# Optimization experiments

Hardware: AMD Instinct MI355X
Metric: run time of the kernel (lower is better)

Reference implementation:

```python
import jax, jax.numpy as jnp
import numpy as np
from jax import lax

V, E, H, L = 32000, 1024, 512, 2
B, S, TL = 32, 128, 63  # batch, src_len, label_len; trg_len = TL+1 = 64
START, PAD = 1, 0
NEG = -1e10


def setup_inputs() -> dict:
    key = jax.random.key(0)
    ks = iter(jax.random.split(key, 40))
    def w(shape):
        return jax.random.normal(next(ks), shape, jnp.float32) * 0.01
    inp = {
        'input_ids': jax.random.randint(next(ks), (B, S), 0, V),
        'attention_mask': jnp.ones((B, S), jnp.int32),
        'labels': jax.random.randint(next(ks), (B, TL), 0, V),
        # encoder params (bidirectional GRU; layer0 input dim E == 2H so stackable)
        'enc_emb': w((V, E)),
        'enc_Wih': w((L, 2, 3 * H, 2 * H)),
        'enc_Whh': w((L, 2, 3 * H, H)),
        'enc_bih': jnp.zeros((L, 2, 3 * H), jnp.float32),
        'enc_bhh': jnp.zeros((L, 2, 3 * H), jnp.float32),
        'fc_W': w((L, H, 2 * H)),
        'fc_b': jnp.zeros((L, H), jnp.float32),
        # attention
        'attn_W': w((H, 3 * H)),
        'attn_b': jnp.zeros((H,), jnp.float32),
        'attn_v': w((H,)),
        # decoder
        'dec_emb': w((V, E)),
        'dec_Wih0': w((3 * H, E + 2 * H)),
        'dec_Wihr': w((L - 1, 3 * H, H)),
        'dec_Whh': w((L, 3 * H, H)),
        'dec_bih': jnp.zeros((L, 3 * H), jnp.float32),
        'dec_bhh': jnp.zeros((L, 3 * H), jnp.float32),
        'out_W': w((V, H + 2 * H + E)),
        'out_b': jnp.zeros((V,), jnp.float32),
    }
    return inp


def gru_cell(x, h, Wih, Whh, bih, bhh):
    gi = x @ Wih.T + bih
    gh = h @ Whh.T + bhh
    i_r, i_z, i_n = jnp.split(gi, 3, axis=-1)
    h_r, h_z, h_n = jnp.split(gh, 3, axis=-1)
    r = jax.nn.sigmoid(i_r + h_r)
    z = jax.nn.sigmoid(i_z + h_z)
    n = jnp.tanh(i_n + r * h_n)
    return (1.0 - z) * n + z * h


def run_dir(x_seq, m_seq, Wih, Whh, bih, bhh, reverse):
    # x_seq: [S,B,D], m_seq: [S,B,1] bool. Emulates pack_padded: hidden freezes
    # past each sequence's length; padded outputs are zero.
    h0 = jnp.zeros((x_seq.shape[1], H), x_seq.dtype)
    def step(h, xm):
        x_t, m_t = xm
        hn = gru_cell(x_t, h, Wih, Whh, bih, bhh)
        return jnp.where(m_t, hn, h), jnp.where(m_t, hn, 0.0)
    hF, outs = lax.scan(step, h0, (x_seq, m_seq), reverse=reverse)
    return outs, hF


def reference(input_ids, attention_mask, labels, enc_emb, enc_Wih, enc_Whh,
              enc_bih, enc_bhh, fc_W, fc_b, attn_W, attn_b, attn_v, dec_emb,
              dec_Wih0, dec_Wihr, dec_Whh, dec_bih, dec_bhh, out_W, out_b):
    src = input_ids.T                                   # [S,B]
    m_sb = (attention_mask.T != 0)[:, :, None]          # [S,B,1]
    x = enc_emb[src]                                    # [S,B,E]
    ff = bf = None
    for l in range(L):
        fo, ff = run_dir(x, m_sb, enc_Wih[l, 0], enc_Whh[l, 0], enc_bih[l, 0], enc_bhh[l, 0], False)
        bo, bf = run_dir(x, m_sb, enc_Wih[l, 1], enc_Whh[l, 1], enc_bih[l, 1], enc_bhh[l, 1], True)
        x = jnp.concatenate([fo, bo], axis=-1)          # [S,B,2H]
    enc_out = x                                         # [S,B,2H]
    fc_in = jnp.concatenate([ff, bf], axis=-1)          # [B,2H]
    hidden = jnp.stack([jnp.tanh(fc_in @ fc_W[l].T + fc_b[l]) for l in range(L)])  # [L,B,H]

    # teacher forcing ratio = 1.0 -> always use target token
    trg = jnp.concatenate([jnp.full((1, B), START, labels.dtype),
                           jnp.where(labels.T == -100, PAD, labels.T)], axis=0)  # [T,B]
    tokens = trg[:-1]                                   # [T-1,B]

    enc_b = enc_out.transpose(1, 0, 2)                  # [B,S,2H]
    mask_b = (attention_mask != 0)                      # [B,S]

    def dec_step(hid, tok):
        emb = dec_emb[tok]                              # [B,E]
        h_top = hid[-1]                                 # [B,H]
        feat = jnp.concatenate(
            [jnp.broadcast_to(h_top[:, None, :], (B, S, H)), enc_b], axis=-1)
        energy = jnp.tanh(feat @ attn_W.T + attn_b)     # [B,S,H]
        scores = jnp.where(mask_b, energy @ attn_v, NEG)
        a = jax.nn.softmax(scores, axis=1)              # [B,S]
        weighted = jnp.einsum('bs,bsd->bd', a, enc_b)   # [B,2H]
        x_l = jnp.concatenate([emb, weighted], axis=-1)
        new_h = []
        h0n = gru_cell(x_l, hid[0], dec_Wih0, dec_Whh[0], dec_bih[0], dec_bhh[0])
        new_h.append(h0n)
        x_l = h0n
        for l in range(1, L):
            hln = gru_cell(x_l, hid[l], dec_Wihr[l - 1], dec_Whh[l], dec_bih[l], dec_bhh[l])
            new_h.append(hln)
            x_l = hln
        pred = jnp.concatenate([x_l, weighted, emb], axis=-1) @ out_W.T + out_b
        return jnp.stack(new_h), pred

    _, preds = lax.scan(dec_step, hidden, tokens)       # [T-1,B,V]
    logits = jnp.concatenate([jnp.zeros((1, B, V), preds.dtype), preds], axis=0)
    return logits.transpose(1, 0, 2)                    # [B,T,V]
```

## Files before the change

### kernel.cpp

```cpp
#include <hip/hip_runtime.h>
#include <hip/hip_bf16.h>

#define V 32000
#define E 1024
#define H 512
#define NL 2
#define B_ 32
#define S_ 128
#define TL_ 63

typedef __attribute__((ext_vector_type(8))) short short8;
typedef __attribute__((ext_vector_type(4))) float f32x4;

__device__ __forceinline__ float sigmoidf_(float x){ return 1.f/(1.f + __expf(-x)); }
__device__ __forceinline__ float fast_tanh(float x){ return 1.f - 2.f/(__expf(2.f*x) + 1.f); }
__device__ __forceinline__ ushort f2bf_(float f){
  uint u = __builtin_bit_cast(uint, f);
  uint r = (u + 0x7FFFu + ((u >> 16) & 1u)) >> 16;
  return (ushort)r;
}

__device__ __forceinline__ float aload(const float* p){
  return __hip_atomic_load(p, __ATOMIC_RELAXED, __HIP_MEMORY_SCOPE_SYSTEM);
}
__device__ __forceinline__ void astore(float* p, float v){
  __hip_atomic_store(p, v, __ATOMIC_RELAXED, __HIP_MEMORY_SCOPE_SYSTEM);
}

__device__ __forceinline__ void gbar(uint* ctr, uint* gen, uint nblk, uint e){
  __syncthreads();
  if (threadIdx.x == 0){
    uint old = __hip_atomic_fetch_add(ctr, 1u, __ATOMIC_RELAXED, __HIP_MEMORY_SCOPE_SYSTEM);
    if (old == e*nblk - 1u){
      __hip_atomic_store(gen, e, __ATOMIC_RELAXED, __HIP_MEMORY_SCOPE_SYSTEM);
    } else {
      while (__hip_atomic_load(gen, __ATOMIC_RELAXED, __HIP_MEMORY_SCOPE_SYSTEM) < e)
        __builtin_amdgcn_s_sleep(2);
    }
  }
  __syncthreads();
}

__global__ __launch_bounds__(256) void embed_enc(const int* __restrict__ ids,
                                                 const float* __restrict__ emb,
                                                 float* __restrict__ X0){
  int row = blockIdx.x;
  int s = row >> 5, b = row & 31;
  int tok = ids[b*S_ + s];
  const float4* src = (const float4*)(emb + (size_t)tok*E);
  float4* dst = (float4*)(X0 + (size_t)row*E);
  dst[threadIdx.x] = src[threadIdx.x];
}

__global__ __launch_bounds__(256) void embed_dec(const int* __restrict__ labels,
                                                 const float* __restrict__ emb,
                                                 float* __restrict__ Feat){
  int row = blockIdx.x;
  int t = row >> 5, b = row & 31;
  int tok = (t == 0) ? 1 : labels[b*TL_ + (t-1)];
  if (tok == -100) tok = 0;
  const float4* src = (const float4*)(emb + (size_t)tok*E);
  float4* dst = (float4*)(Feat + (size_t)row*2560 + 1536);
  dst[threadIdx.x] = src[threadIdx.x];
}

__global__ __launch_bounds__(256) void gemm_f32(
    const float* __restrict__ A, int lda,
    const float* __restrict__ B, int ldb,
    const float* __restrict__ bias,
    float* __restrict__ C, int ldc,
    int M, int N, int K)
{
  __shared__ float As[8][132];
  __shared__ float Bs[8][132];
  int tid = threadIdx.x;
  int row0 = blockIdx.x*128, col0 = blockIdx.y*128;
  int lr = tid >> 1;
  int lk = (tid & 1) * 4;
  int ar = row0 + lr; if (ar > M-1) ar = M-1;
  const float* Ap = A + (size_t)ar*lda + lk;
  const float* Bp = B + (size_t)(col0 + lr)*ldb + lk;
  int tx = tid & 15, ty = tid >> 4;
  float acc[8][8];
  #pragma unroll
  for (int i=0;i<8;i++){
    #pragma unroll
    for (int j=0;j<8;j++) acc[i][j]=0.f;
  }
  for (int k0 = 0; k0 < K; k0 += 8){
    float4 a = *(const float4*)(Ap + k0);
    float4 b = *(const float4*)(Bp + k0);
    __syncthreads();
    As[lk+0][lr]=a.x; As[lk+1][lr]=a.y; As[lk+2][lr]=a.z; As[lk+3][lr]=a.w;
    Bs[lk+0][lr]=b.x; Bs[lk+1][lr]=b.y; Bs[lk+2][lr]=b.z; Bs[lk+3][lr]=b.w;
    __syncthreads();
    #pragma unroll
    for (int k=0;k<8;k++){
      float av[8], bv[8];
      *(float4*)&av[0] = *(const float4*)&As[k][ty*8];
      *(float4*)&av[4] = *(const float4*)&As[k][ty*8+4];
      *(float4*)&bv[0] = *(const float4*)&Bs[k][tx*8];
      *(float4*)&bv[4] = *(const float4*)&Bs[k][tx*8+4];
      #pragma unroll
      for (int i=0;i<8;i++){
        #pragma unroll
        for (int j=0;j<8;j++) acc[i][j] += av[i]*bv[j];
      }
    }
  }
  #pragma unroll
  for (int i=0;i<8;i++){
    int r = row0 + ty*8 + i;
    if (r < M){
      float* Cp = C + (size_t)r*ldc + col0 + tx*8;
      #pragma unroll
      for (int j=0;j<8;j++) Cp[j] = acc[i][j] + bias[col0 + tx*8 + j];
    }
  }
}

__global__ __launch_bounds__(256) void enc_layer(
    const float* __restrict__ GIf, const float* __restrict__ GIbk,
    const float* __restrict__ Whh, const float* __restrict__ bhh,
    const int* __restrict__ amask,
    float* __restrict__ hFa, float* __restrict__ hFb,
    float* __restrict__ hBa, float* __restrict__ hBb,
    float* __restrict__ Xout, uint* __restrict__ barbase)
{
  int dir  = blockIdx.x >> 7;
  int rr   = blockIdx.x & 127;
  int bg   = rr >> 4;
  int jblk = rr & 15;
  uint* z   = barbase + (size_t)(dir*8 + bg)*512;
  uint* ctr = z; uint* gen = z + 1;
  const float* GI = dir ? GIbk : GIf;
  const float* W  = Whh + (size_t)dir*1536*512;
  const float* bh = bhh + dir*1536;
  float* hA = dir ? hBa : hFa;
  float* hB = dir ? hBb : hFb;
  int tid = threadIdx.x;
  int bl = tid & 3, jl = (tid >> 2) & 31, kh = tid >> 7;
  int j = jblk*32 + jl;
  int b = bg*4 + bl;
  const float* w0 = W + (size_t)j*512        + kh*256;
  const float* w1 = W + (size_t)(j+512)*512  + kh*256;
  const float* w2 = W + (size_t)(j+1024)*512 + kh*256;
  float b0 = bh[j], b1 = bh[j+512], b2 = bh[j+1024];
  __shared__ float hS[4][512];
  __shared__ float red[256*3];
  uint e = 1;
  for (int step = 0; step < S_; step++){
    const float* hin = (step & 1) ? hB : hA;
    float*       hout= (step & 1) ? hA : hB;
    int t = dir ? (S_-1 - step) : step;
    for (int i = tid; i < 2048; i += 256){
      int bs = i >> 9, k = i & 511;
      hS[bs][k] = aload(hin + (size_t)(bg*4 + bs)*512 + k);
    }
    __syncthreads();
    float s0=0.f, s1=0.f, s2=0.f;
    #pragma unroll 8
    for (int k=0;k<256;k+=4){
      float x0 = hS[bl][kh*256 + k];
      float x1 = hS[bl][kh*256 + k + 1];
      float x2 = hS[bl][kh*256 + k + 2];
      float x3 = hS[bl][kh*256 + k + 3];
      float4 v0 = *(const float4*)(w0+k);
      float4 v1 = *(const float4*)(w1+k);
      float4 v2 = *(const float4*)(w2+k);
      s0 += x0*v0.x + x1*v0.y + x2*v0.z + x3*v0.w;
      s1 += x0*v1.x + x1*v1.y + x2*v1.z + x3*v1.w;
      s2 += x0*v2.x + x1*v2.y + x2*v2.z + x3*v2.w;
    }
    red[tid*3+0]=s0; red[tid*3+1]=s1; red[tid*3+2]=s2;
    __syncthreads();
    if (kh == 0){
      float sr = s0 + red[(tid+128)*3+0];
      float sz = s1 + red[(tid+128)*3+1];
      float sn = s2 + red[(tid+128)*3+2];
      const float* gi = GI + ((size_t)t*32 + b)*1536;
      float r = sigmoidf_(gi[j]      + sr + b0);
      float z_ = sigmoidf_(gi[j+512]  + sz + b1);
      float n = fast_tanh(gi[j+1024] + r*(sn + b2));
      float hold = hS[bl][j];
      float hn = (1.f - z_)*n + z_*hold;
      int m = amask[b*S_ + t];
      astore(hout + (size_t)b*512 + j, m ? hn : hold);
      Xout[((size_t)t*32 + b)*1024 + dir*512 + j] = m ? hn : 0.f;
    }
    gbar(ctr, gen, 16, e); e++;
  }
}

__global__ __launch_bounds__(256) void fc_init(
    const float* __restrict__ hF, const float* __restrict__ hB,
    const float* __restrict__ fcW, const float* __restrict__ fcb,
    float* __restrict__ h0T, float* __restrict__ h1T)
{
  int idx = blockIdx.x*256 + threadIdx.x;
  int l = idx >> 14;
  int b = (idx >> 9) & 31;
  int jj = idx & 511;
  const float* w = fcW + ((size_t)(l*512 + jj))*1024;
  const float* hf = hF + (size_t)b*512;
  const float* hb = hB + (size_t)b*512;
  float s = fcb[l*512 + jj];
  #pragma unroll 4
  for (int k=0;k<512;k+=4){
    float4 wv = *(const float4*)(w+k);
    s += hf[k+0]*wv.x + hf[k+1]*wv.y + hf[k+2]*wv.z + hf[k+3]*wv.w;
    float4 wv2 = *(const float4*)(w+512+k);
    s += hb[k+0]*wv2.x + hb[k+1]*wv2.y + hb[k+2]*wv2.z + hb[k+3]*wv2.w;
  }
  (l ? h1T : h0T)[jj*32 + b] = fast_tanh(s);
}

__global__ __launch_bounds__(256) void dec_loop(
    const float* __restrict__ ENC,  const float* __restrict__ Eenc,
    const float* __restrict__ aW,   const float* __restrict__ av,
    const int* __restrict__ amask,
    const float* __restrict__ GI0,  const float* __restrict__ Wih0,
    const float* __restrict__ Wihr, const float* __restrict__ Whh,
    const float* __restrict__ bih,  const float* __restrict__ bhh,
    float* __restrict__ h0a, float* __restrict__ h0b,
    float* __restrict__ h1a, float* __restrict__ h1b,
    float* __restrict__ wgtT, float* __restrict__ part,
    float* __restrict__ Feat, uint* __restrict__ barbase)
{
  uint* ctr = barbase;
  uint* gen = ctr + 1;
  __shared__ float eeS[128*64];
  __shared__ float encS[128*128];
  __shared__ float sm[1600];
  int tid = threadIdx.x;
  int bid = blockIdx.x;
  const float* Whh1 = Whh + (size_t)1536*512;
  const float* bih1 = bih + 1536;
  const float* bhh1 = bhh + 1536;
  uint e = 1;

  int bP = bid >> 3, kg = bid & 7;
  int wv = tid >> 6, ln = tid & 63;
  int jl2 = tid & 127, kh2 = tid >> 7;
  int jcol = kg*128 + jl2;

  for (int i = tid; i < 128*64; i += 256){
    int s = i >> 6, kk = i & 63;
    eeS[i] = Eenc[((size_t)s*32 + bP)*512 + kg*64 + kk];
  }
  for (int i = tid; i < 128*128; i += 256){
    int s = i >> 7, j2 = i & 127;
    encS[i] = ENC[((size_t)s*32 + bP)*1024 + kg*128 + j2];
  }
  __syncthreads();

  for (int t = 0; t < TL_; t++){
    const float* h0cur = (t & 1) ? h0b : h0a;  float* h0nxt = (t & 1) ? h0a : h0b;
    const float* h1cur = (t & 1) ? h1b : h1a;  float* h1nxt = (t & 1) ? h1a : h1b;

    {
      float hreg[8];
      #pragma unroll
      for (int q=0;q<8;q++) hreg[q] = aload(h1cur + (ln*8+q)*32 + bP);
      float avreg = av[kg*64 + ln];
      float* pre_s = sm;
      #pragma unroll 4
      for (int i=0;i<16;i++){
        int k = kg*64 + wv*16 + i;
        const float* wr = aW + (size_t)k*1536 + ln*8;
        float4 u0 = *(const float4*)wr;
        float4 u1 = *(const float4*)(wr+4);
        float p = u0.x*hreg[0]+u0.y*hreg[1]+u0.z*hreg[2]+u0.w*hreg[3]
                + u1.x*hreg[4]+u1.y*hreg[5]+u1.z*hreg[6]+u1.w*hreg[7];
        #pragma unroll
        for (int off=32; off>0; off>>=1) p += __shfl_xor(p, off);
        if (ln == i) pre_s[wv*16+i] = p;
      }
      __syncthreads();
      float myPre = pre_s[ln];
      for (int si=0; si<32; si++){
        int s = wv*32 + si;
        float ee = eeS[s*64 + ln];
        float v = fast_tanh(myPre + ee) * avreg;
        #pragma unroll
        for (int off=32; off>0; off>>=1) v += __shfl_xor(v, off);
        if (ln == 0) astore(&part[(bP*8+kg)*128 + s], v);
      }
    }
    gbar(ctr, gen, 256, e); e++;

    {
      float* praw = sm;
      float* sa   = sm + 1024;
      float* aw   = sm + 1152;
      float* red2 = sm + 1280;
      float* sv   = sm + 1536;
      #pragma unroll
      for (int q=0;q<4;q++) praw[tid*4+q] = aload(&part[bP*1024 + tid*4+q]);
      __syncthreads();
      if (tid < 128){
        float s8 = 0.f;
        #pragma unroll
        for (int kg2=0;kg2<8;kg2++) s8 += praw[kg2*128 + tid];
        sa[tid] = amask[bP*S_ + tid] ? s8 : -1e10f;
      }
      __syncthreads();
      if (tid < 64){
        float m0 = fmaxf(sa[tid], sa[tid+64]);
        #pragma unroll
        for (int off=32; off>0; off>>=1) m0 = fmaxf(m0, __shfl_xor(m0, off));
        float e0 = __expf(sa[tid]-m0), e1 = __expf(sa[tid+64]-m0);
        aw[tid] = e0; aw[tid+64] = e1;
        float ss = e0 + e1;
        #pragma unroll
        for (int off=32; off>0; off>>=1) ss += __shfl_xor(ss, off);
        if (tid == 0) sv[0] = ss;
      }
      __syncthreads();
      float inv = 1.f / sv[0];
      float p = 0.f;
      #pragma unroll
      for (int s=0;s<64;s++) p += aw[kh2*64+s] * encS[(kh2*64+s)*128 + jl2];
      red2[jl2*2+kh2] = p;
      __syncthreads();
      if (kh2 == 0){
        float wvv = (red2[jl2*2] + red2[jl2*2+1]) * inv;
        astore(&wgtT[jcol*32 + bP], wvv);
        Feat[((size_t)t*32 + bP)*2560 + 512 + jcol] = wvv;
      }
    }
    gbar(ctr, gen, 256, e); e++;

    {
      int b = tid & 31, kq = (tid >> 5) & 3, jl = tid >> 7;
      int jj = bid*2 + jl;
      const float* u0 = Wih0 + (size_t)jj*2048        + 1024 + kq*256;
      const float* u1 = Wih0 + (size_t)(jj+512)*2048  + 1024 + kq*256;
      const float* u2 = Wih0 + (size_t)(jj+1024)*2048 + 1024 + kq*256;
      const float* xT = wgtT + (size_t)(kq*256)*32 + b;
      float a0=0.f, a1=0.f, a2=0.f;
      #pragma unroll 8
      for (int k=0;k<256;k+=4){
        float x0=aload(xT+(k+0)*32), x1=aload(xT+(k+1)*32);
        float x2=aload(xT+(k+2)*32), x3=aload(xT+(k+3)*32);
        float4 v0=*(const float4*)(u0+k);
        float4 v1=*(const float4*)(u1+k);
        float4 v2=*(const float4*)(u2+k);
        a0 += x0*v0.x + x1*v0.y + x2*v0.z + x3*v0.w;
        a1 += x0*v1.x + x1*v1.y + x2*v1.z + x3*v1.w;
        a2 += x0*v2.x + x1*v2.y + x2*v2.z + x3*v2.w;
      }
      const float* w0 = Whh + (size_t)jj*512        + kq*128;
      const float* w1 = Whh + (size_t)(jj+512)*512  + kq*128;
      const float* w2 = Whh + (size_t)(jj+1024)*512 + kq*128;
      const float* hT = h0cur + (size_t)(kq*128)*32 + b;
      float s0=0.f, s1=0.f, s2=0.f;
      #pragma unroll 8
      for (int k=0;k<128;k+=4){
        float x0=aload(hT+(k+0)*32), x1=aload(hT+(k+1)*32);
        float x2=aload(hT+(k+2)*32), x3=aload(hT+(k+3)*32);
        float4 v0=*(const float4*)(w0+k);
        float4 v1=*(const float4*)(w1+k);
        float4 v2=*(const float4*)(w2+k);
        s0 += x0*v0.x + x1*v0.y + x2*v0.z + x3*v0.w;
        s1 += x0*v1.x + x1*v1.y + x2*v1.z + x3*v1.w;
        s2 += x0*v2.x + x1*v2.y + x2*v2.z + x3*v2.w;
      }
      float* red = sm;
      int ridx = ((jl*4 + kq)*32 + b)*4;
      red[ridx+0] = a0 + s0;
      red[ridx+1] = a1 + s1;
      red[ridx+2] = a2;
      red[ridx+3] = s2;
      __syncthreads();
      if (kq == 0){
        float P0=0.f, P1=0.f, P2=0.f, P3=0.f;
        #pragma unroll
        for (int q=0;q<4;q++){
          int ri = ((jl*4 + q)*32 + b)*4;
          P0 += red[ri+0]; P1 += red[ri+1]; P2 += red[ri+2]; P3 += red[ri+3];
        }
        const float* gi = GI0 + ((size_t)t*32 + b)*1536;
        float r = sigmoidf_(gi[jj]      + P0 + bhh[jj]);
        float z_ = sigmoidf_(gi[jj+512]  + P1 + bhh[jj+512]);
        float n = fast_tanh(gi[jj+1024] + P2 + r*(P3 + bhh[jj+1024]));
        float hold = aload(h0cur + jj*32 + b);
        astore(h0nxt + jj*32 + b, (1.f - z_)*n + z_*hold);
      }
    }
    gbar(ctr, gen, 256, e); e++;

    {
      int b = tid & 31, kq = (tid >> 5) & 3, jl = tid >> 7;
      int jj = bid*2 + jl;
      const float* i0 = Wihr + (size_t)jj*512        + kq*128;
      const float* i1 = Wihr + (size_t)(jj+512)*512  + kq*128;
      const float* i2 = Wihr + (size_t)(jj+1024)*512 + kq*128;
      const float* xT = h0nxt + (size_t)(kq*128)*32 + b;
      float a0=0.f, a1=0.f, a2=0.f;
      #pragma unroll 8
      for (int k=0;k<128;k+=4){
        float x0=aload(xT+(k+0)*32), x1=aload(xT+(k+1)*32);
        float x2=aload(xT+(k+2)*32), x3=aload(xT+(k+3)*32);
        float4 v0=*(const float4*)(i0+k);
        float4 v1=*(const float4*)(i1+k);
        float4 v2=*(const float4*)(i2+k);
        a0 += x0*v0.x + x1*v0.y + x2*v0.z + x3*v0.w;
        a1 += x0*v1.x + x1*v1.y + x2*v1.z + x3*v1.w;
        a2 += x0*v2.x + x1*v2.y + x2*v2.z + x3*v2.w;
      }
      const float* w0 = Whh1 + (size_t)jj*512        + kq*128;
      const float* w1 = Whh1 + (size_t)(jj+512)*512  + kq*128;
      const float* w2 = Whh1 + (size_t)(jj+1024)*512 + kq*128;
      const float* hT = h1cur + (size_t)(kq*128)*32 + b;
      float s0=0.f, s1=0.f, s2=0.f;
      #pragma unroll 8
      for (int k=0;k<128;k+=4){
        float x0=aload(hT+(k+0)*32), x1=aload(hT+(k+1)*32);
        float x2=aload(hT+(k+2)*32), x3=aload(hT+(k+3)*32);
        float4 v0=*(const float4*)(w0+k);
        float4 v1=*(const float4*)(w1+k);
        float4 v2=*(const float4*)(w2+k);
        s0 += x0*v0.x + x1*v0.y + x2*v0.z + x3*v0.w;
        s1 += x0*v1.x + x1*v1.y + x2*v1.z + x3*v1.w;
        s2 += x0*v2.x + x1*v2.y + x2*v2.z + x3*v2.w;
      }
      float* red = sm;
      int ridx = ((jl*4 + kq)*32 + b)*4;
      red[ridx+0] = a0 + s0;
      red[ridx+1] = a1 + s1;
      red[ridx+2] = a2;
      red[ridx+3] = s2;
      __syncthreads();
      if (kq == 0){
        float P0=0.f, P1=0.f, P2=0.f, P3=0.f;
        #pragma unroll
        for (int q=0;q<4;q++){
          int ri = ((jl*4 + q)*32 + b)*4;
          P0 += red[ri+0]; P1 += red[ri+1]; P2 += red[ri+2]; P3 += red[ri+3];
        }
        float r = sigmoidf_(P0 + bih1[jj]      + bhh1[jj]);
        float z_ = sigmoidf_(P1 + bih1[jj+512]  + bhh1[jj+512]);
        float n = fast_tanh(P2 + bih1[jj+1024] + r*(P3 + bhh1[jj+1024]));
        float hold = aload(h1cur + jj*32 + b);
        float hn = (1.f - z_)*n + z_*hold;
        astore(h1nxt + jj*32 + b, hn);
        Feat[((size_t)t*32 + b)*2560 + jj] = hn;
      }
    }
    gbar(ctr, gen, 256, e); e++;
  }
}

__global__ __launch_bounds__(256) void zero_t0(float* __restrict__ out){
  int idx = blockIdx.x*256 + threadIdx.x;
  if (idx < 32*V){
    int b = idx / V, v = idx - b*V;
    out[(size_t)b*64*V + v] = 0.f;
  }
}

__global__ __launch_bounds__(256) void out_gemm(
    const float* __restrict__ A,
    const float* __restrict__ Bw,
    const float* __restrict__ bias,
    float* __restrict__ out)
{
  __shared__ ushort As[4][129][8];
  __shared__ ushort Bs[4][129][8];
  int tid = threadIdx.x;
  int lane = tid & 63, wid = tid >> 6;
  int row0 = blockIdx.x*128, col0 = blockIdx.y*128;
  int sr = tid >> 1;
  int s0 = (tid & 1) * 2;
  int sk = (tid & 1) * 16;
  int arow = row0 + sr; if (arow > 2015) arow = 2015;
  const float* Ap = A + (size_t)arow*2560 + sk;
  const float* Bp = Bw + (size_t)(col0 + sr)*2560 + sk;
  int wr = (wid >> 1)*64, wc = (wid & 1)*64;
  int fr = lane & 15, slot = lane >> 4;
  f32x4 acc[4][4];
  #pragma unroll
  for (int m=0;m<4;m++){
    #pragma unroll
    for (int n=0;n<4;n++) acc[m][n] = (f32x4){0.f,0.f,0.f,0.f};
  }
  for (int k0 = 0; k0 < 2560; k0 += 32){
    float4 a0 = *(const float4*)(Ap + k0);
    float4 a1 = *(const float4*)(Ap + k0 + 4);
    float4 a2 = *(const float4*)(Ap + k0 + 8);
    float4 a3 = *(const float4*)(Ap + k0 + 12);
    float4 b0 = *(const float4*)(Bp + k0);
    float4 b1 = *(const float4*)(Bp + k0 + 4);
    float4 b2 = *(const float4*)(Bp + k0 + 8);
    float4 b3 = *(const float4*)(Bp + k0 + 12);
    __syncthreads();
    short8 va, va2, vb, vb2;
    va[0]=f2bf_(a0.x); va[1]=f2bf_(a0.y); va[2]=f2bf_(a0.z); va[3]=f2bf_(a0.w);
    va[4]=f2bf_(a1.x); va[5]=f2bf_(a1.y); va[6]=f2bf_(a1.z); va[7]=f2bf_(a1.w);
    va2[0]=f2bf_(a2.x); va2[1]=f2bf_(a2.y); va2[2]=f2bf_(a2.z); va2[3]=f2bf_(a2.w);
    va2[4]=f2bf_(a3.x); va2[5]=f2bf_(a3.y); va2[6]=f2bf_(a3.z); va2[7]=f2bf_(a3.w);
    vb[0]=f2bf_(b0.x); vb[1]=f2bf_(b0.y); vb[2]=f2bf_(b0.z); vb[3]=f2bf_(b0.w);
    vb[4]=f2bf_(b1.x); vb[5]=f2bf_(b1.y); vb[6]=f2bf_(b1.z); vb[7]=f2bf_(b1.w);
    vb2[0]=f2bf_(b2.x); vb2[1]=f2bf_(b2.y); vb2[2]=f2bf_(b2.z); vb2[3]=f2bf_(b2.w);
    vb2[4]=f2bf_(b3.x); vb2[5]=f2bf_(b3.y); vb2[6]=f2bf_(b3.z); vb2[7]=f2bf_(b3.w);
    *(short8*)&As[s0  ][sr][0] = va;
    *(short8*)&As[s0+1][sr][0] = va2;
    *(short8*)&Bs[s0  ][sr][0] = vb;
    *(short8*)&Bs[s0+1][sr][0] = vb2;
    __syncthreads();
    short8 af[4], bfr[4];
    #pragma unroll
    for (int m=0;m<4;m++) af[m]  = *(const short8*)&As[slot][wr + m*16 + fr][0];
    #pragma unroll
    for (int n=0;n<4;n++) bfr[n] = *(const short8*)&Bs[slot][wc + n*16 + fr][0];
    #pragma unroll
    for (int m=0;m<4;m++){
      #pragma unroll
      for (int n=0;n<4;n++)
        acc[m][n] = __builtin_amdgcn_mfma_f32_16x16x32_bf16(af[m], bfr[n], acc[m][n], 0, 0, 0);
    }
  }
  int cb = lane & 15, rb = (lane >> 4)*4;
  #pragma unroll
  for (int m=0;m<4;m++){
    #pragma unroll
    for (int n=0;n<4;n++){
      int c = col0 + wc + n*16 + cb;
      float bi = bias[c];
      #pragma unroll
      for (int j=0;j<4;j++){
        int r = row0 + wr + m*16 + rb + j;
        if (r < 2016){
          int bb = r & 31, tt = r >> 5;
          out[((size_t)bb*64 + tt + 1)*V + c] = acc[m][n][j] + bi;
        }
      }
    }
  }
}

extern "C" void kernel_launch(void* const* d_in, const int* in_sizes, int n_in,
                              void* d_out, int out_size, void* d_ws, size_t ws_size,
                              hipStream_t stream) {
  (void)in_sizes; (void)n_in; (void)out_size; (void)ws_size;
  const int*   ids    = (const int*)d_in[0];
  const int*   amask  = (const int*)d_in[1];
  const int*   labels = (const int*)d_in[2];
  const float* enc_emb= (const float*)d_in[3];
  const float* eWih   = (const float*)d_in[4];
  const float* eWhh   = (const float*)d_in[5];
  const float* ebih   = (const float*)d_in[6];
  const float* ebhh   = (const float*)d_in[7];
  const float* fcW    = (const float*)d_in[8];
  const float* fcb    = (const float*)d_in[9];
  const float* aW     = (const float*)d_in[10];
  const float* ab     = (const float*)d_in[11];
  const float* av     = (const float*)d_in[12];
  const float* dec_emb= (const float*)d_in[13];
  const float* dWih0  = (const float*)d_in[14];
  const float* dWihr  = (const float*)d_in[15];
  const float* dWhh   = (const float*)d_in[16];
  const float* dbih   = (const float*)d_in[17];
  const float* dbhh   = (const float*)d_in[18];
  const float* outW   = (const float*)d_in[19];
  const float* outb   = (const float*)d_in[20];
  float* out = (float*)d_out;

  uint*  bar = (uint*)d_ws;
  float* ws  = (float*)d_ws + 20480;
  float* X0  = ws;
  float* X1  = X0  + (size_t)4096*1024;
  float* ENC = X1  + (size_t)4096*1024;
  float* GIa = ENC + (size_t)4096*1024;
  float* GIb = GIa + (size_t)4096*1536;
  float* Eenc= GIb + (size_t)4096*1536;
  float* GI0 = Eenc+ (size_t)4096*512;
  float* Feat= GI0 + (size_t)2016*1536;
  float* hp  = Feat+ (size_t)2016*2560;
  float* hFa = hp;             float* hFb = hFa + 32*512;
  float* hBa = hFb + 32*512;   float* hBb = hBa + 32*512;
  float* h0a = hBb + 32*512;   float* h0b = h0a + 32*512;
  float* h1a = h0b + 32*512;   float* h1b = h1a + 32*512;
  float* wgtT = h1b + 32*512;
  float* part = wgtT + 32*1024;

  hipMemsetAsync(bar, 0, 20480*sizeof(uint), stream);

  embed_enc<<<4096, 256, 0, stream>>>(ids, enc_emb, X0);
  for (int l = 0; l < NL; l++){
    const float* Xin = l ? X1 : X0;
    float* Xout = l ? ENC : X1;
    hipMemsetAsync(hFa, 0, 32*512*sizeof(float), stream);
    hipMemsetAsync(hBa, 0, 32*512*sizeof(float), stream);
    gemm_f32<<<dim3(32,12),256,0,stream>>>(Xin, 1024, eWih + (size_t)(l*2+0)*1536*1024, 1024,
        ebih + (l*2+0)*1536, GIa, 1536, 4096, 1536, 1024);
    gemm_f32<<<dim3(32,12),256,0,stream>>>(Xin, 1024, eWih + (size_t)(l*2+1)*1536*1024, 1024,
        ebih + (l*2+1)*1536, GIb, 1536, 4096, 1536, 1024);
    {
      const float* gia = GIa; const float* gib = GIb;
      const float* whhp = eWhh + (size_t)l*2*1536*512;
      const float* bhhp = ebhh + (size_t)l*2*1536;
      uint* eb = bar + (size_t)l*8192;
      void* args[] = {(void*)&gia, (void*)&gib, (void*)&whhp, (void*)&bhhp,
                      (void*)&amask, (void*)&hFa, (void*)&hFb, (void*)&hBa,
                      (void*)&hBb, (void*)&Xout, (void*)&eb};
      hipLaunchCooperativeKernel((const void*)enc_layer, dim3(256), dim3(256), args, 0, stream);
    }
  }
  fc_init<<<128,256,0,stream>>>(hFa, hBa, fcW, fcb, h0a, h1a);
  gemm_f32<<<dim3(32,4),256,0,stream>>>(ENC, 1024, aW + 512, 1536, ab, Eenc, 512, 4096, 512, 1024);
  embed_dec<<<2016,256,0,stream>>>(labels, dec_emb, Feat);
  gemm_f32<<<dim3(16,12),256,0,stream>>>(Feat + 1536, 2560, dWih0, 2048, dbih, GI0, 1536, 2016, 1536, 1024);
  {
    const float* encp = ENC; const float* eencp = Eenc; const float* gi0p = GI0;
    float* featp = Feat;
    uint* db = bar + 16384;
    void* args[] = {(void*)&encp, (void*)&eencp, (void*)&aW, (void*)&av,
                    (void*)&amask, (void*)&gi0p, (void*)&dWih0, (void*)&dWihr,
                    (void*)&dWhh, (void*)&dbih, (void*)&dbhh,
                    (void*)&h0a, (void*)&h0b, (void*)&h1a, (void*)&h1b,
                    (void*)&wgtT, (void*)&part, (void*)&featp, (void*)&db};
    hipLaunchCooperativeKernel((const void*)dec_loop, dim3(256), dim3(256), args, 0, stream);
  }
  zero_t0<<<4000,256,0,stream>>>(out);
  out_gemm<<<dim3(16,250),256,0,stream>>>(Feat, outW, outb, out);
}
```

Measured before the change: 10.58 ms.

## Use per-timestep buffers, plain loads, and per-batch barrier in decoder loop

The decoder's ping-pong hidden, weighted-context and partial-score buffers become per-timestep ring buffers placed in the now-unused encoder workspace. Because each address is written only once, reads can be plain cached loads instead of system-scope atomic loads. The first grid-wide barrier after the attention partial scores becomes a barrier over only the 8 blocks that share a batch row. The risk is that plain loads may hit stale cache lines; this is safe only if gbar's fences and the write-once addressing keep caches coherent.

```diff
diff --git a/kernel.cpp b/kernel.cpp
--- a/kernel.cpp
+++ b/kernel.cpp
@@ -212,7 +212,8 @@
     float4 wv2 = *(const float4*)(w+512+k);
     s += hb[k+0]*wv2.x + hb[k+1]*wv2.y + hb[k+2]*wv2.z + hb[k+3]*wv2.w;
   }
-  (l ? h1T : h0T)[jj*32 + b] = fast_tanh(s);
+  __hip_atomic_store(&(l ? h1T : h0T)[jj*32 + b], fast_tanh(s),
+                     __ATOMIC_RELAXED, __HIP_MEMORY_SCOPE_SYSTEM);
 }
 
 __global__ __launch_bounds__(256) void dec_loop(
@@ -222,9 +223,8 @@
     const float* __restrict__ GI0,  const float* __restrict__ Wih0,
     const float* __restrict__ Wihr, const float* __restrict__ Whh,
     const float* __restrict__ bih,  const float* __restrict__ bhh,
-    float* __restrict__ h0a, float* __restrict__ h0b,
-    float* __restrict__ h1a, float* __restrict__ h1b,
-    float* __restrict__ wgtT, float* __restrict__ part,
+    float* __restrict__ h0R, float* __restrict__ h1R,
+    float* __restrict__ wgtR, float* __restrict__ partR,
     float* __restrict__ Feat, uint* __restrict__ barbase)
 {
   uint* ctr = barbase;
@@ -237,9 +237,12 @@
   const float* Whh1 = Whh + (size_t)1536*512;
   const float* bih1 = bih + 1536;
   const float* bhh1 = bhh + 1536;
-  uint e = 1;
+  uint ef = 1;
+  uint ez = 1;
 
   int bP = bid >> 3, kg = bid & 7;
+  uint* zctr = barbase + 64 + bP*32;
+  uint* zgen = zctr + 1;
   int wv = tid >> 6, ln = tid & 63;
   int jl2 = tid & 127, kh2 = tid >> 7;
   int jcol = kg*128 + jl2;
@@ -255,13 +258,17 @@
   __syncthreads();
 
   for (int t = 0; t < TL_; t++){
-    const float* h0cur = (t & 1) ? h0b : h0a;  float* h0nxt = (t & 1) ? h0a : h0b;
-    const float* h1cur = (t & 1) ? h1b : h1a;  float* h1nxt = (t & 1) ? h1a : h1b;
+    const float* h0cur = h0R + (size_t)t*16384;
+    float*       h0nxt = h0R + (size_t)(t+1)*16384;
+    const float* h1cur = h1R + (size_t)t*16384;
+    float*       h1nxt = h1R + (size_t)(t+1)*16384;
+    float*       wgtT  = wgtR + (size_t)t*32768;
+    float*       part  = partR + (size_t)t*32768;
 
     {
       float hreg[8];
       #pragma unroll
-      for (int q=0;q<8;q++) hreg[q] = aload(h1cur + (ln*8+q)*32 + bP);
+      for (int q=0;q<8;q++) hreg[q] = h1cur[(ln*8+q)*32 + bP];
       float avreg = av[kg*64 + ln];
       float* pre_s = sm;
       #pragma unroll 4
@@ -287,7 +294,7 @@
         if (ln == 0) astore(&part[(bP*8+kg)*128 + s], v);
       }
     }
-    gbar(ctr, gen, 256, e); e++;
+    gbar(zctr, zgen, 8, ez); ez++;
 
     {
       float* praw = sm;
@@ -296,7 +303,7 @@
       float* red2 = sm + 1280;
       float* sv   = sm + 1536;
       #pragma unroll
-      for (int q=0;q<4;q++) praw[tid*4+q] = aload(&part[bP*1024 + tid*4+q]);
+      for (int q=0;q<4;q++) praw[tid*4+q] = part[bP*1024 + tid*4+q];
       __syncthreads();
       if (tid < 128){
         float s8 = 0.f;
@@ -329,7 +336,7 @@
         Feat[((size_t)t*32 + bP)*2560 + 512 + jcol] = wvv;
       }
     }
-    gbar(ctr, gen, 256, e); e++;
+    gbar(ctr, gen, 256, ef); ef++;
 
     {
       int b = tid & 31, kq = (tid >> 5) & 3, jl = tid >> 7;
@@ -341,8 +348,8 @@
       float a0=0.f, a1=0.f, a2=0.f;
       #pragma unroll 8
       for (int k=0;k<256;k+=4){
-        float x0=aload(xT+(k+0)*32), x1=aload(xT+(k+1)*32);
-        float x2=aload(xT+(k+2)*32), x3=aload(xT+(k+3)*32);
+        float x0=xT[(k+0)*32], x1=xT[(k+1)*32];
+        float x2=xT[(k+2)*32], x3=xT[(k+3)*32];
         float4 v0=*(const float4*)(u0+k);
         float4 v1=*(const float4*)(u1+k);
         float4 v2=*(const float4*)(u2+k);
@@ -357,8 +364,8 @@
       float s0=0.f, s1=0.f, s2=0.f;
       #pragma unroll 8
       for (int k=0;k<128;k+=4){
-        float x0=aload(hT+(k+0)*32), x1=aload(hT+(k+1)*32);
-        float x2=aload(hT+(k+2)*32), x3=aload(hT+(k+3)*32);
+        float x0=hT[(k+0)*32], x1=hT[(k+1)*32];
+        float x2=hT[(k+2)*32], x3=hT[(k+3)*32];
         float4 v0=*(const float4*)(w0+k);
         float4 v1=*(const float4*)(w1+k);
         float4 v2=*(const float4*)(w2+k);
@@ -384,11 +391,11 @@
         float r = sigmoidf_(gi[jj]      + P0 + bhh[jj]);
         float z_ = sigmoidf_(gi[jj+512]  + P1 + bhh[jj+512]);
         float n = fast_tanh(gi[jj+1024] + P2 + r*(P3 + bhh[jj+1024]));
-        float hold = aload(h0cur + jj*32 + b);
+        float hold = h0cur[jj*32 + b];
         astore(h0nxt + jj*32 + b, (1.f - z_)*n + z_*hold);
       }
     }
-    gbar(ctr, gen, 256, e); e++;
+    gbar(ctr, gen, 256, ef); ef++;
 
     {
       int b = tid & 31, kq = (tid >> 5) & 3, jl = tid >> 7;
@@ -400,8 +407,8 @@
       float a0=0.f, a1=0.f, a2=0.f;
       #pragma unroll 8
       for (int k=0;k<128;k+=4){
-        float x0=aload(xT+(k+0)*32), x1=aload(xT+(k+1)*32);
-        float x2=aload(xT+(k+2)*32), x3=aload(xT+(k+3)*32);
+        float x0=xT[(k+0)*32], x1=xT[(k+1)*32];
+        float x2=xT[(k+2)*32], x3=xT[(k+3)*32];
         float4 v0=*(const float4*)(i0+k);
         float4 v1=*(const float4*)(i1+k);
         float4 v2=*(const float4*)(i2+k);
@@ -416,8 +423,8 @@
       float s0=0.f, s1=0.f, s2=0.f;
       #pragma unroll 8
       for (int k=0;k<128;k+=4){
-        float x0=aload(hT+(k+0)*32), x1=aload(hT+(k+1)*32);
-        float x2=aload(hT+(k+2)*32), x3=aload(hT+(k+3)*32);
+        float x0=hT[(k+0)*32], x1=hT[(k+1)*32];
+        float x2=hT[(k+2)*32], x3=hT[(k+3)*32];
         float4 v0=*(const float4*)(w0+k);
         float4 v1=*(const float4*)(w1+k);
         float4 v2=*(const float4*)(w2+k);
@@ -442,13 +449,13 @@
         float r = sigmoidf_(P0 + bih1[jj]      + bhh1[jj]);
         float z_ = sigmoidf_(P1 + bih1[jj+512]  + bhh1[jj+512]);
         float n = fast_tanh(P2 + bih1[jj+1024] + r*(P3 + bhh1[jj+1024]));
-        float hold = aload(h1cur + jj*32 + b);
+        float hold = h1cur[jj*32 + b];
         float hn = (1.f - z_)*n + z_*hold;
         astore(h1nxt + jj*32 + b, hn);
         Feat[((size_t)t*32 + b)*2560 + jj] = hn;
       }
     }
-    gbar(ctr, gen, 256, e); e++;
+    gbar(ctr, gen, 256, ef); ef++;
   }
 }
 
@@ -580,10 +587,10 @@
   float* hp  = Feat+ (size_t)2016*2560;
   float* hFa = hp;             float* hFb = hFa + 32*512;
   float* hBa = hFb + 32*512;   float* hBb = hBa + 32*512;
-  float* h0a = hBb + 32*512;   float* h0b = h0a + 32*512;
-  float* h1a = h0b + 32*512;   float* h1b = h1a + 32*512;
-  float* wgtT = h1b + 32*512;
-  float* part = wgtT + 32*1024;
+  float* wgtR  = X0;
+  float* partR = X0 + (size_t)63*32768;
+  float* h0R   = X1;
+  float* h1R   = X1 + (size_t)64*16384;
 
   hipMemsetAsync(bar, 0, 20480*sizeof(uint), stream);
 
@@ -608,7 +615,7 @@
       hipLaunchCooperativeKernel((const void*)enc_layer, dim3(256), dim3(256), args, 0, stream);
     }
   }
-  fc_init<<<128,256,0,stream>>>(hFa, hBa, fcW, fcb, h0a, h1a);
+  fc_init<<<128,256,0,stream>>>(hFa, hBa, fcW, fcb, h0R, h1R);
   gemm_f32<<<dim3(32,4),256,0,stream>>>(ENC, 1024, aW + 512, 1536, ab, Eenc, 512, 4096, 512, 1024);
   embed_dec<<<2016,256,0,stream>>>(labels, dec_emb, Feat);
   gemm_f32<<<dim3(16,12),256,0,stream>>>(Feat + 1536, 2560, dWih0, 2048, dbih, GI0, 1536, 2016, 1536, 1024);
@@ -619,8 +626,8 @@
     void* args[] = {(void*)&encp, (void*)&eencp, (void*)&aW, (void*)&av,
                     (void*)&amask, (void*)&gi0p, (void*)&dWih0, (void*)&dWihr,
                     (void*)&dWhh, (void*)&dbih, (void*)&dbhh,
-                    (void*)&h0a, (void*)&h0b, (void*)&h1a, (void*)&h1b,
-                    (void*)&wgtT, (void*)&part, (void*)&featp, (void*)&db};
+                    (void*)&h0R, (void*)&h1R, (void*)&wgtR, (void*)&partR,
+                    (void*)&featp, (void*)&db};
     hipLaunchCooperativeKernel((const void*)dec_loop, dim3(256), dim3(256), args, 0, stream);
   }
   zero_t0<<<4000,256,0,stream>>>(out);
```

Result: slower. 10.99 ms (+4.0%).
